# Optimization experiments

Measured on AMD Instinct MI355X. Metric: run time of the kernel, lower is better.

## Reference

```python
import jax, jax.numpy as jnp
import numpy as np

N, IN_FEAT, OUT_FEAT = 16384, 1024, 4096


def setup_inputs() -> dict:
    key = jax.random.key(0)
    k_x, k_m, k_w, k_b = jax.random.split(key, 4)
    x = jax.random.normal(k_x, (N, IN_FEAT), dtype=jnp.float32)
    amask = jax.random.randint(k_m, (N,), 0, 2, dtype=jnp.int32)
    # nn.Linear(in_feat, out_feat): weight [out, in], bias [out]
    W = jax.random.normal(k_w, (OUT_FEAT, IN_FEAT), dtype=jnp.float32) * (1.0 / np.sqrt(IN_FEAT))
    b = jax.random.normal(k_b, (OUT_FEAT,), dtype=jnp.float32) * 0.001
    return {"x": x, "amask": amask, "W": W, "b": b}


def reference(x, amask, W, b):
    # Torch code gathers rows where amask != 0, applies linear (+identity act),
    # and scatters results back into a zero [N, out_feat] tensor. Equivalent
    # dense-math (jit-friendly, no data-dependent shapes): compute the linear
    # on all rows and zero out unmasked rows. Same output values.
    y = jnp.einsum('ni,oi->no', x, W) + b  # [N, out_feat]
    keep = (amask != 0)[:, None]
    return jnp.where(keep, y, jnp.zeros((), dtype=x.dtype))
```

## Files before the change

kernel.cpp:

```cpp
#include <hip/hip_runtime.h>
#include <hip/hip_bf16.h>
#include <stdint.h>

#define N_ROWS 16384
#define K_DIM  1024
#define N_OUT  4096

typedef __attribute__((ext_vector_type(8))) short short8;
typedef __attribute__((ext_vector_type(4))) float f32x4;
typedef __attribute__((ext_vector_type(4))) __bf16 bf16x4;

__global__ void cvt_kernel(const float* __restrict__ in, __bf16* __restrict__ out, int n4) {
    int stride = gridDim.x * blockDim.x;
    for (int i = blockIdx.x * blockDim.x + threadIdx.x; i < n4; i += stride) {
        float4 v = reinterpret_cast<const float4*>(in)[i];
        bf16x4 o;
        o[0] = (__bf16)v.x; o[1] = (__bf16)v.y; o[2] = (__bf16)v.z; o[3] = (__bf16)v.w;
        reinterpret_cast<bf16x4*>(out)[i] = o;
    }
}

__global__ __launch_bounds__(256) void cvt_gather_kernel(
    const float* __restrict__ x, const int* __restrict__ idx,
    const int* __restrict__ count, __bf16* __restrict__ xb) {
    const int cnt = count[0];
    const int t = threadIdx.x;
    for (int j = blockIdx.x; j < cnt; j += gridDim.x) {
        const int row = idx[j];
        float4 v = reinterpret_cast<const float4*>(x + (size_t)row * K_DIM)[t];
        bf16x4 o;
        o[0] = (__bf16)v.x; o[1] = (__bf16)v.y; o[2] = (__bf16)v.z; o[3] = (__bf16)v.w;
        reinterpret_cast<bf16x4*>(xb + (size_t)j * K_DIM)[t] = o;
    }
}

__global__ __launch_bounds__(1024) void scan_kernel(const int* __restrict__ amask,
                                                    int* __restrict__ idx,
                                                    int* __restrict__ zidx,
                                                    int* __restrict__ count) {
    __shared__ int sc[1024];
    const int t = threadIdx.x;
    const int base = t * 16;
    int mk[16];
#pragma unroll
    for (int g = 0; g < 4; ++g) {
        int4 m4 = reinterpret_cast<const int4*>(amask + base)[g];
        mk[g*4+0] = m4.x; mk[g*4+1] = m4.y; mk[g*4+2] = m4.z; mk[g*4+3] = m4.w;
    }
    int c = 0;
#pragma unroll
    for (int i = 0; i < 16; ++i) c += (mk[i] != 0) ? 1 : 0;
    int v = c;
    sc[t] = v;
    __syncthreads();
    for (int off = 1; off < 1024; off <<= 1) {
        int u = (t >= off) ? sc[t - off] : 0;
        __syncthreads();
        v += u; sc[t] = v;
        __syncthreads();
    }
    int b  = v - c;
    int zb = base - b;
#pragma unroll
    for (int i = 0; i < 16; ++i) {
        int r = base + i;
        if (mk[i] != 0) idx[b++] = r; else zidx[zb++] = r;
    }
    if (t == 1023) count[0] = v;
}


#define GLL(SRC, DSTOFF)                                                       \
    __builtin_amdgcn_global_load_lds(                                          \
        (const __attribute__((address_space(1))) void*)(SRC),                  \
        (__attribute__((address_space(3))) void*)(ldsc + (DSTOFF)), 16, 0, 0)

__global__ __launch_bounds__(256) void gemm_kernel(
    const __bf16* __restrict__ A,
    const __bf16* __restrict__ B,
    const float*  __restrict__ bias,
    const int*    __restrict__ idx,
    const int*    __restrict__ zidx,
    const int*    __restrict__ count,
    float*        __restrict__ out)
{
    __shared__ short lds_all[8192];

    const int t  = threadIdx.x;
    const int l  = t & 63;
    const int w  = t >> 6;
    const int wm = w >> 1;
    const int wn = w & 1;

    const int cnt = count[0];
    const int aT  = (cnt + 127) >> 7;
    const int q   = (aT + 7) >> 3;

    const int bid = blockIdx.x;
    const int xcd = bid & 7;
    const int c   = bid >> 3;
    const int pre = min(xcd * q, aT);
    int own = aT - pre; if (own > q) own = q; if (own < 0) own = 0;
    const int h   = own * 32;

    const int hb   = (c * h) >> 9;
    const bool hvy = (((c + 1) * h) >> 9) > hb;

    if (!hvy) {
        const int trank = c - hb;
        const int tr  = (512 * xcd - 32 * pre) + trank;
        const int tnt = tr & 31;
        const int zsl = tr >> 5;
        const int zt  = 128 - aT;
        const int nz  = N_ROWS - cnt;
        const int rpz = (nz + zt - 1) / zt;
        const int lo  = zsl * rpz;
        const int hi0 = lo + rpz;
        const int hi  = hi0 < nz ? hi0 : nz;
        const int n0z = tnt * 128;
        const float2 zf = make_float2(0.f, 0.f);
        for (int i = lo + w; i < hi; i += 4) {
            const int row = zidx[i];
            float2* p = reinterpret_cast<float2*>(out + (size_t)row * N_OUT + n0z);
            p[l] = zf;
        }
        return;
    }

    const int tm = pre + (hb % own);
    const int tn = hb / own;
    const int m0 = tm * 128;
    const int n0 = tn * 128;

    const int srow = t >> 2;
    const int sk8  = (t & 3) * 8;
    const __bf16* pA0 = A + (size_t)(m0 + srow) * K_DIM + sk8;
    const __bf16* pA1 = pA0 + (size_t)64 * K_DIM;
    const __bf16* pB0 = B + (size_t)(n0 + srow) * K_DIM + sk8;
    const __bf16* pB1 = pB0 + (size_t)64 * K_DIM;
    char* ldsc = (char*)lds_all;

    const int lr = l & 15;
    const int lk = (l >> 4) * 8;

    f32x4 acc[4][4] = {};

    for (int k0 = 0; k0 < K_DIM; k0 += 32) {
        GLL(pA0 + k0, t * 16);
        GLL(pA1 + k0, 4096 + t * 16);
        GLL(pB0 + k0, 8192 + t * 16);
        GLL(pB1 + k0, 12288 + t * 16);
        __syncthreads();

        short8 af[4], bf[4];
#pragma unroll
        for (int mi = 0; mi < 4; ++mi)
            af[mi] = *(const short8*)(lds_all + (wm*64 + mi*16 + lr)*32 + lk);
#pragma unroll
        for (int ni = 0; ni < 4; ++ni)
            bf[ni] = *(const short8*)(lds_all + 4096 + (wn*64 + ni*16 + lr)*32 + lk);

#pragma unroll
        for (int mi = 0; mi < 4; ++mi)
#pragma unroll
            for (int ni = 0; ni < 4; ++ni)
                acc[mi][ni] = __builtin_amdgcn_mfma_f32_16x16x32_bf16(
                    af[mi], bf[ni], acc[mi][ni], 0, 0, 0);
        __syncthreads();
    }

    const int lq = l >> 4;
    float bv[4];
#pragma unroll
    for (int ni = 0; ni < 4; ++ni) bv[ni] = bias[n0 + wn*64 + ni*16 + lr];

#pragma unroll
    for (int mi = 0; mi < 4; ++mi) {
        const int slot0 = m0 + wm*64 + mi*16 + lq*4;
        int rowid[4]; bool val[4];
#pragma unroll
        for (int r = 0; r < 4; ++r) {
            const int s = slot0 + r;
            val[r] = (s < cnt);
            rowid[r] = val[r] ? idx[s] : 0;
        }
#pragma unroll
        for (int ni = 0; ni < 4; ++ni) {
            const int cc = n0 + wn*64 + ni*16 + lr;
#pragma unroll
            for (int r = 0; r < 4; ++r)
                if (val[r]) out[(size_t)rowid[r] * N_OUT + cc] = acc[mi][ni][r] + bv[ni];
        }
    }
}

__global__ void naive_kernel(const float* __restrict__ x, const float* __restrict__ W,
                             const float* __restrict__ bias, const int* __restrict__ amask,
                             float* __restrict__ out) {
    int c = blockIdx.x * blockDim.x + threadIdx.x;
    int r = blockIdx.y;
    if (c >= N_OUT) return;
    if (amask[r] == 0) { out[(size_t)r * N_OUT + c] = 0.0f; return; }
    const float* xr = x + (size_t)r * K_DIM;
    const float* wr = W + (size_t)c * K_DIM;
    float s = 0.0f;
    for (int k = 0; k < K_DIM; ++k) s += xr[k] * wr[k];
    out[(size_t)r * N_OUT + c] = s + bias[c];
}

extern "C" void kernel_launch(void* const* d_in, const int* in_sizes, int n_in,
                              void* d_out, int out_size, void* d_ws, size_t ws_size,
                              hipStream_t stream) {
    const float* x     = (const float*)d_in[0];
    const int*   amask = (const int*)d_in[1];
    const float* W     = (const float*)d_in[2];
    const float* bias  = (const float*)d_in[3];
    float*       out   = (float*)d_out;

    const size_t xb_bytes = (size_t)N_ROWS * K_DIM * 2;
    const size_t wb_bytes = (size_t)N_OUT  * K_DIM * 2;
    const size_t idx_bytes = (size_t)N_ROWS * 4;
    const size_t need = xb_bytes + wb_bytes + 2 * idx_bytes + 256;

    if (ws_size < need) {
        dim3 g((N_OUT + 255) / 256, N_ROWS);
        naive_kernel<<<g, 256, 0, stream>>>(x, W, bias, amask, out);
        return;
    }

    __bf16* xb   = (__bf16*)d_ws;
    __bf16* wb   = (__bf16*)((char*)d_ws + xb_bytes);
    int*    idx  = (int*)((char*)d_ws + xb_bytes + wb_bytes);
    int*    zidx = idx + N_ROWS;
    int*    cnt  = zidx + N_ROWS;

    scan_kernel<<<1, 1024, 0, stream>>>(amask, idx, zidx, cnt);
    cvt_gather_kernel<<<2048, 256, 0, stream>>>(x, idx, cnt, xb);
    cvt_kernel<<<1024, 256, 0, stream>>>(W, wb, N_OUT * K_DIM / 4);

    gemm_kernel<<<4096, 256, 0, stream>>>(xb, wb, bias, idx, zidx, cnt, out);
}
```

Measured before the change: 182.6 us.

## Fuse mask scan with weight conversion and zero whole rows per block

Result: faster. 175.0 us (-4.2%).

```diff
diff --git a/kernel.cpp b/kernel.cpp
--- a/kernel.cpp
+++ b/kernel.cpp
@@ -10,14 +10,49 @@
 typedef __attribute__((ext_vector_type(4))) float f32x4;
 typedef __attribute__((ext_vector_type(4))) __bf16 bf16x4;
 
-__global__ void cvt_kernel(const float* __restrict__ in, __bf16* __restrict__ out, int n4) {
-    int stride = gridDim.x * blockDim.x;
-    for (int i = blockIdx.x * blockDim.x + threadIdx.x; i < n4; i += stride) {
-        float4 v = reinterpret_cast<const float4*>(in)[i];
+__global__ __launch_bounds__(1024) void prep_kernel(
+    const int*   __restrict__ amask,
+    const float* __restrict__ W,
+    int* __restrict__ idx, int* __restrict__ zidx, int* __restrict__ count,
+    __bf16* __restrict__ wb)
+{
+    const int t = threadIdx.x;
+    if (blockIdx.x != 0) {
+        const int i = (blockIdx.x - 1) * 1024 + t;
+        float4 v = reinterpret_cast<const float4*>(W)[i];
         bf16x4 o;
         o[0] = (__bf16)v.x; o[1] = (__bf16)v.y; o[2] = (__bf16)v.z; o[3] = (__bf16)v.w;
-        reinterpret_cast<bf16x4*>(out)[i] = o;
-    }
+        reinterpret_cast<bf16x4*>(wb)[i] = o;
+        return;
+    }
+    __shared__ int sc[1024];
+    const int base = t * 16;
+    int mk[16];
+#pragma unroll
+    for (int g = 0; g < 4; ++g) {
+        int4 m4 = reinterpret_cast<const int4*>(amask + base)[g];
+        mk[g*4+0] = m4.x; mk[g*4+1] = m4.y; mk[g*4+2] = m4.z; mk[g*4+3] = m4.w;
+    }
+    int c = 0;
+#pragma unroll
+    for (int i = 0; i < 16; ++i) c += (mk[i] != 0) ? 1 : 0;
+    int v = c;
+    sc[t] = v;
+    __syncthreads();
+    for (int off = 1; off < 1024; off <<= 1) {
+        int u = (t >= off) ? sc[t - off] : 0;
+        __syncthreads();
+        v += u; sc[t] = v;
+        __syncthreads();
+    }
+    int b  = v - c;
+    int zb = base - b;
+#pragma unroll
+    for (int i = 0; i < 16; ++i) {
+        int r = base + i;
+        if (mk[i] != 0) idx[b++] = r; else zidx[zb++] = r;
+    }
+    if (t == 1023) count[0] = v;
 }
 
 __global__ __launch_bounds__(256) void cvt_gather_kernel(
@@ -34,41 +69,6 @@
     }
 }
 
-__global__ __launch_bounds__(1024) void scan_kernel(const int* __restrict__ amask,
-                                                    int* __restrict__ idx,
-                                                    int* __restrict__ zidx,
-                                                    int* __restrict__ count) {
-    __shared__ int sc[1024];
-    const int t = threadIdx.x;
-    const int base = t * 16;
-    int mk[16];
-#pragma unroll
-    for (int g = 0; g < 4; ++g) {
-        int4 m4 = reinterpret_cast<const int4*>(amask + base)[g];
-        mk[g*4+0] = m4.x; mk[g*4+1] = m4.y; mk[g*4+2] = m4.z; mk[g*4+3] = m4.w;
-    }
-    int c = 0;
-#pragma unroll
-    for (int i = 0; i < 16; ++i) c += (mk[i] != 0) ? 1 : 0;
-    int v = c;
-    sc[t] = v;
-    __syncthreads();
-    for (int off = 1; off < 1024; off <<= 1) {
-        int u = (t >= off) ? sc[t - off] : 0;
-        __syncthreads();
-        v += u; sc[t] = v;
-        __syncthreads();
-    }
-    int b  = v - c;
-    int zb = base - b;
-#pragma unroll
-    for (int i = 0; i < 16; ++i) {
-        int r = base + i;
-        if (mk[i] != 0) idx[b++] = r; else zidx[zb++] = r;
-    }
-    if (t == 1023) count[0] = v;
-}
-
 
 #define GLL(SRC, DSTOFF)                                                       \
     __builtin_amdgcn_global_load_lds(                                          \
@@ -107,22 +107,20 @@
     const bool hvy = (((c + 1) * h) >> 9) > hb;
 
     if (!hvy) {
-        const int trank = c - hb;
-        const int tr  = (512 * xcd - 32 * pre) + trank;
-        const int tnt = tr & 31;
-        const int zsl = tr >> 5;
-        const int zt  = 128 - aT;
-        const int nz  = N_ROWS - cnt;
-        const int rpz = (nz + zt - 1) / zt;
-        const int lo  = zsl * rpz;
-        const int hi0 = lo + rpz;
-        const int hi  = hi0 < nz ? hi0 : nz;
-        const int n0z = tnt * 128;
-        const float2 zf = make_float2(0.f, 0.f);
+        const int tr    = (512 * xcd - 32 * pre) + (c - hb);
+        const int ntriv = 4096 - aT * 32;
+        const int nz    = N_ROWS - cnt;
+        const int rpz   = (nz + ntriv - 1) / ntriv;
+        const int lo    = tr * rpz;
+        const int hi0   = lo + rpz;
+        const int hi    = hi0 < nz ? hi0 : nz;
+        const float4 zf = make_float4(0.f, 0.f, 0.f, 0.f);
         for (int i = lo + w; i < hi; i += 4) {
             const int row = zidx[i];
-            float2* p = reinterpret_cast<float2*>(out + (size_t)row * N_OUT + n0z);
-            p[l] = zf;
+            float4* p = reinterpret_cast<float4*>(out + (size_t)row * N_OUT);
+#pragma unroll
+            for (int u = 0; u < 16; ++u)
+                p[u * 64 + l] = zf;
         }
         return;
     }
@@ -234,9 +232,8 @@
     int*    zidx = idx + N_ROWS;
     int*    cnt  = zidx + N_ROWS;
 
-    scan_kernel<<<1, 1024, 0, stream>>>(amask, idx, zidx, cnt);
+    prep_kernel<<<1025, 1024, 0, stream>>>(amask, W, idx, zidx, cnt, wb);
     cvt_gather_kernel<<<2048, 256, 0, stream>>>(x, idx, cnt, xb);
-    cvt_kernel<<<1024, 256, 0, stream>>>(W, wb, N_OUT * K_DIM / 4);
 
     gemm_kernel<<<4096, 256, 0, stream>>>(xb, wb, bias, idx, zidx, cnt, out);
 }
```
